# Optimization experiments

Hardware: AMD Instinct MI355X
Metric: run time of the kernel (lower is better)

The kernel has to match this reference:

```python
import jax, jax.numpy as jnp
import numpy as np

NUM_HEADS = 4
D_MODEL = 256
HEAD_DIM = D_MODEL // NUM_HEADS  # 64
B, N = 8, 2048


def _proj(x, W, b):
    # Conv1d with kernel_size=1 == pointwise linear over channel dim
    # x: [B, C_in, N], W: [C_out, C_in], b: [C_out]
    return jnp.einsum('oi,bin->bon', W, x) + b[None, :, None]


def setup_inputs() -> dict:
    key = jax.random.key(0)
    ks = jax.random.split(key, 11)
    s = 1.0 / np.sqrt(D_MODEL)
    return {
        'query': jax.random.normal(ks[0], (B, D_MODEL, N), jnp.float32),
        'key':   jax.random.normal(ks[1], (B, D_MODEL, N), jnp.float32),
        'value': jax.random.normal(ks[2], (B, D_MODEL, N), jnp.float32),
        'Wq': jax.random.normal(ks[3], (D_MODEL, D_MODEL), jnp.float32) * s,
        'bq': jax.random.normal(ks[4], (D_MODEL,), jnp.float32) * 0.01,
        'Wk': jax.random.normal(ks[5], (D_MODEL, D_MODEL), jnp.float32) * s,
        'bk': jax.random.normal(ks[6], (D_MODEL,), jnp.float32) * 0.01,
        'Wv': jax.random.normal(ks[7], (D_MODEL, D_MODEL), jnp.float32) * s,
        'bv': jax.random.normal(ks[8], (D_MODEL,), jnp.float32) * 0.01,
        'Wm': jax.random.normal(ks[9], (D_MODEL, D_MODEL), jnp.float32) * s,
        'bm': jax.random.normal(ks[10], (D_MODEL,), jnp.float32) * 0.01,
    }


def reference(query, key, value, Wq, bq, Wk, bk, Wv, bv, Wm, bm):
    b = query.shape[0]
    # project then split channels into (head_dim, num_heads): [B, d, h, N]
    q = _proj(query, Wq, bq).reshape(b, HEAD_DIM, NUM_HEADS, -1)
    k = _proj(key,   Wk, bk).reshape(b, HEAD_DIM, NUM_HEADS, -1)
    v = _proj(value, Wv, bv).reshape(b, HEAD_DIM, NUM_HEADS, -1)
    scale = 1.0 / jnp.sqrt(jnp.asarray(HEAD_DIM, q.dtype))
    scores = jnp.einsum('bdhn,bdhm->bhnm', q, k) * scale  # [B,H,N,N]
    prob = jax.nn.softmax(scores, axis=-1)
    x = jnp.einsum('bhnm,bdhm->bdhn', prob, v)  # [B,d,H,N]
    x = x.reshape(b, HEAD_DIM * NUM_HEADS, -1)  # [B, d_model, N]
    return _proj(x, Wm, bm)
```

## Files before the change

### kernel.cpp

```cpp
#include <hip/hip_runtime.h>
#include <math.h>


constexpr int BATCH  = 8;
constexpr int DMODEL = 256;
constexpr int SEQ    = 2048;
constexpr int HDIM   = 64;
constexpr int TN     = 128;
constexpr int TM     = 64;
constexpr int NJT    = SEQ / TM;

typedef _Float16 half4_t __attribute__((ext_vector_type(4)));
typedef _Float16 half8_t __attribute__((ext_vector_type(8)));
typedef float    float4_t __attribute__((ext_vector_type(4)));

static __device__ __forceinline__ void ld16_lds(const void* g, void* l) {
    __builtin_amdgcn_global_load_lds(
        (const __attribute__((address_space(1))) unsigned*)g,
        (__attribute__((address_space(3))) unsigned*)l, 16, 0, 0);
}

__global__ __launch_bounds__(256)
void prep_w(const float* __restrict__ Wq, const float* __restrict__ Wk,
            const float* __restrict__ Wv, const float* __restrict__ Wm,
            _Float16* __restrict__ wf)
{
    const int which = blockIdx.y;
    const float* src = which == 0 ? Wq : which == 1 ? Wk : which == 2 ? Wv : Wm;
    const int i = (blockIdx.x * 256 + threadIdx.x) * 4;
    const float4 v = *(const float4*)&src[i];
    half4_t o; o[0] = v.x; o[1] = v.y; o[2] = v.z; o[3] = v.w;
    *(half4_t*)&wf[(size_t)which * DMODEL * DMODEL + i] = o;
}

__global__ __launch_bounds__(256, 3)
void gemm_qkv(const _Float16* __restrict__ wf, const float* __restrict__ bq,
              const float* __restrict__ bk, const float* __restrict__ bv,
              const float* __restrict__ Xq, const float* __restrict__ Xk,
              const float* __restrict__ Xv, _Float16* __restrict__ qT,
              _Float16* __restrict__ kT, _Float16* __restrict__ vT)
{
    const int n0 = blockIdx.x * 64;
    const int proj = blockIdx.y >> 3, b = blockIdx.y & 7;
    const _Float16* W    = wf + (size_t)proj * DMODEL * DMODEL;
    const float*    bias = proj == 0 ? bq : proj == 1 ? bk : bv;
    const float*    X    = (proj == 0 ? Xq : proj == 1 ? Xk : Xv)
                           + (size_t)b * DMODEL * SEQ;
    const float qs = (proj == 0) ? 0.18033688011112042f : 1.0f;

    __shared__ __align__(16) char lds[50432];
    float*    T  = (float*)lds;
    _Float16* Xs = (_Float16*)(lds + 16640);
    _Float16* Tw = (_Float16*)lds;

    const int tid = threadIdx.x, tn = tid & 15, tc = tid >> 4;

    #pragma unroll
    for (int cc = 0; cc < 4; ++cc) {
        __syncthreads();
        #pragma unroll
        for (int i = 0; i < 4; ++i) {
            const int c = tc + 16 * i;
            const float4 v = *(const float4*)&X[(size_t)(cc * 64 + c) * SEQ + n0 + tn * 4];
            T[c * 65 + tn * 4 + 0] = v.x; T[c * 65 + tn * 4 + 1] = v.y;
            T[c * 65 + tn * 4 + 2] = v.z; T[c * 65 + tn * 4 + 3] = v.w;
        }
        __syncthreads();
        #pragma unroll
        for (int i = 0; i < 4; ++i) {
            const int n = tc + 16 * i;
            half4_t h4;
            #pragma unroll
            for (int j = 0; j < 4; ++j) h4[j] = (_Float16)T[(tn * 4 + j) * 65 + n];
            *(half4_t*)&Xs[n * 264 + cc * 64 + tn * 4] = h4;
        }
    }
    __syncthreads();

    const int w = tid >> 6, lane = tid & 63;
    const int lm = lane & 15, g = lane >> 4, g8 = g * 8;
    const int cw0 = w * 64;

    float4_t acc[4][4];
    #pragma unroll
    for (int mt = 0; mt < 4; ++mt)
        #pragma unroll
        for (int nt = 0; nt < 4; ++nt) acc[mt][nt] = (float4_t){0.f, 0.f, 0.f, 0.f};

    #pragma unroll
    for (int k0 = 0; k0 < DMODEL; k0 += 64) {
        half8_t a[4][2], bb[4][2];
        #pragma unroll
        for (int mt = 0; mt < 4; ++mt)
            #pragma unroll
            for (int kd = 0; kd < 2; ++kd)
                a[mt][kd] = *(const half8_t*)&W[(size_t)(cw0 + mt * 16 + lm) * DMODEL
                                                + k0 + kd * 32 + g8];
        #pragma unroll
        for (int nt = 0; nt < 4; ++nt)
            #pragma unroll
            for (int kd = 0; kd < 2; ++kd)
                bb[nt][kd] = *(const half8_t*)&Xs[(nt * 16 + lm) * 264
                                                  + k0 + kd * 32 + g8];
        #pragma unroll
        for (int kd = 0; kd < 2; ++kd)
            #pragma unroll
            for (int mt = 0; mt < 4; ++mt)
                #pragma unroll
                for (int nt = 0; nt < 4; ++nt)
                    acc[mt][nt] = __builtin_amdgcn_mfma_f32_16x16x32_f16(
                        a[mt][kd], bb[nt][kd], acc[mt][nt], 0, 0, 0);
    }
    __syncthreads();

    #pragma unroll
    for (int mt = 0; mt < 4; ++mt) {
        const float4 b4 = *(const float4*)&bias[cw0 + mt * 16 + g * 4];
        const float bb4[4] = {b4.x, b4.y, b4.z, b4.w};
        #pragma unroll
        for (int nt = 0; nt < 4; ++nt) {
            half4_t pk;
            #pragma unroll
            for (int r = 0; r < 4; ++r)
                pk[r] = (_Float16)((acc[mt][nt][r] + bb4[r]) * qs);
            *(half4_t*)&Tw[((w * 64 + nt * 16 + lm)) * 68 + mt * 16 + g * 4] = pk;
        }
    }

    if (proj < 2) {
        _Float16* dst = (proj == 0 ? qT : kT);
        const int h2 = lane >> 4, lml = lane & 15;
        #pragma unroll
        for (int it = 0; it < 4; ++it) {
            const int nl = it * 16 + lml;
            const int hs = (nl & 3) | (((nl >> 3) & 1) << 2);
            #pragma unroll
            for (int dc = 0; dc < 2; ++dc) {
                half8_t ch;
                #pragma unroll
                for (int e = 0; e < 8; ++e)
                    ch[e] = Tw[(w * 64 + nl) * 68 + 4 * (dc * 8 + e) + h2];
                const int chunk = (w * 2 + dc) ^ hs;
                *(half8_t*)&dst[((size_t)(b * 4 + h2) * SEQ + n0 + nl) * HDIM
                                + chunk * 8] = ch;
            }
        }
    } else {
        const int hh = lane & 3, dl = (lane >> 2) & 15;
        const int d = w * 16 + dl;
        const size_t rowbase =
            (((size_t)(b * 4 + hh) * NJT + (n0 >> 6)) * HDIM + d) * (size_t)TM;
        #pragma unroll
        for (int jc = 0; jc < 8; ++jc) {
            half8_t ch;
            #pragma unroll
            for (int e = 0; e < 8; ++e)
                ch[e] = Tw[(w * 64 + jc * 8 + e) * 68 + 4 * dl + hh];
            *(half8_t*)&vT[rowbase + ((jc ^ (dl & 7)) << 3)] = ch;
        }
    }
}

__global__ __launch_bounds__(256, 4)
void attn_f16(const _Float16* __restrict__ qT, const _Float16* __restrict__ kT,
              const _Float16* __restrict__ vT, _Float16* __restrict__ xa,
              _Float16* __restrict__ xb, float* __restrict__ rs)
{
    const int lid = blockIdx.x;
    const int work = (lid & 7) * 128 + (lid >> 3);
    const int bh = work >> 5, b = bh >> 2, h = bh & 3;
    const int jh = (work >> 4) & 1;
    const int ib = work & 15;
    const int tid = threadIdx.x, wid = tid >> 6, lane = tid & 63;
    const int lm = lane & 15, g = lane >> 4;
    const int i0 = ib * TN + wid * 32;

    __shared__ _Float16 Kb[2][TM * HDIM];
    __shared__ _Float16 Vb[2][TM * HDIM];

    const int hq = (lm & 3) | (((lm >> 3) & 1) << 2);
    const int hk = (lm & 3) | (((lm >> 2) & 1) << 2);
    const int rbase = 8 * (lm >> 2) + (lm & 3);

    half8_t bq[2][2];
    const _Float16* qbase = qT + (size_t)bh * SEQ * HDIM;
    #pragma unroll
    for (int rt = 0; rt < 2; ++rt)
        #pragma unroll
        for (int kd = 0; kd < 2; ++kd) {
            const int row = i0 + rt * 16 + lm;
            bq[rt][kd] = *(const half8_t*)(qbase + (size_t)row * HDIM
                                           + (((kd * 4 + g) ^ hq) << 3));
        }

    const char* kt = (const char*)(kT + ((size_t)bh * SEQ + jh * (SEQ / 2)) * HDIM);
    const char* vt = (const char*)(vT + ((size_t)bh * NJT + jh * 16) * TM * HDIM);

    float4_t o[2][4];
    float rsum[2][2] = {{0.f, 0.f}, {0.f, 0.f}};
    #pragma unroll
    for (int rt = 0; rt < 2; ++rt)
        #pragma unroll
        for (int dt = 0; dt < 4; ++dt) o[rt][dt] = (float4_t){0.f, 0.f, 0.f, 0.f};

    #define STAGE(jt, bu)                                                     \
        {                                                                     \
            const char* kg = kt + (size_t)(jt) * 8192;                        \
            const char* vg = vt + (size_t)(jt) * 8192;                        \
            _Pragma("unroll")                                                 \
            for (int p = 0; p < 2; ++p) {                                     \
                const int c = wid + p * 4;                                    \
                ld16_lds(kg + c * 1024 + lane * 16, (char*)&Kb[bu][0] + c * 1024); \
                ld16_lds(vg + c * 1024 + lane * 16, (char*)&Vb[bu][0] + c * 1024); \
            }                                                                 \
        }

    STAGE(0, 0);
    __syncthreads();

    for (int jt = 0; jt < 16; ++jt) {
        const int cur = jt & 1;
        if (jt + 1 < 16) STAGE(jt + 1, cur ^ 1);

        float4_t s[2][2][2];
        #pragma unroll
        for (int jb = 0; jb < 2; ++jb)
            #pragma unroll
            for (int u = 0; u < 2; ++u)
                #pragma unroll
                for (int rt = 0; rt < 2; ++rt)
                    s[jb][u][rt] = (float4_t){0.f, 0.f, 0.f, 0.f};
        #pragma unroll
        for (int kd = 0; kd < 2; ++kd)
            #pragma unroll
            for (int jb = 0; jb < 2; ++jb)
                #pragma unroll
                for (int u = 0; u < 2; ++u) {
                    const int jrow = jb * 32 + rbase + 4 * u;
                    const half8_t fk = *(const half8_t*)
                        &Kb[cur][jrow * HDIM + (((kd * 4 + g) ^ hk) << 3)];
                    #pragma unroll
                    for (int rt = 0; rt < 2; ++rt)
                        s[jb][u][rt] = __builtin_amdgcn_mfma_f32_16x16x32_f16(
                            fk, bq[rt][kd], s[jb][u][rt], 0, 0, 0);
                }

        half8_t ap[2][2];
        #pragma unroll
        for (int jb = 0; jb < 2; ++jb)
            #pragma unroll
            for (int rt = 0; rt < 2; ++rt) {
                half8_t p;
                #pragma unroll
                for (int r = 0; r < 4; ++r) {
                    const float e0 = __builtin_amdgcn_exp2f(s[jb][0][rt][r]);
                    const float e1 = __builtin_amdgcn_exp2f(s[jb][1][rt][r]);
                    rsum[jb][rt] += e0;
                    rsum[jb][rt] += e1;
                    p[r]     = (_Float16)e0;
                    p[r + 4] = (_Float16)e1;
                }
                ap[jb][rt] = p;
            }

        #pragma unroll
        for (int jb = 0; jb < 2; ++jb)
            #pragma unroll
            for (int dt = 0; dt < 4; ++dt) {
                const int d = dt * 16 + lm;
                const half8_t fv = *(const half8_t*)
                    &Vb[cur][d * TM + (((jb * 4 + g) ^ (lm & 7)) << 3)];
                #pragma unroll
                for (int rt = 0; rt < 2; ++rt)
                    o[rt][dt] = __builtin_amdgcn_mfma_f32_16x16x32_f16(
                        ap[jb][rt], fv, o[rt][dt], 0, 0, 0);
            }
        __syncthreads();
    }

    _Float16* xp = jh ? xb : xa;
    #pragma unroll
    for (int rt = 0; rt < 2; ++rt)
        #pragma unroll
        for (int dt = 0; dt < 4; ++dt) {
            const int c = 4 * (dt * 16 + lm) + h;
            #pragma unroll
            for (int r = 0; r < 4; ++r) {
                const int n = i0 + rt * 16 + 4 * g + r;
                xp[((size_t)b * SEQ + n) * DMODEL + c] = (_Float16)o[rt][dt][r];
            }
        }
    #pragma unroll
    for (int rt = 0; rt < 2; ++rt) {
        float v = rsum[0][rt] + rsum[1][rt];
        v += __shfl_xor(v, 16);
        v += __shfl_xor(v, 32);
        if (g == 0)
            rs[((size_t)jh * 32 + bh) * SEQ + i0 + rt * 16 + lm] = v;
    }
    #undef STAGE
}

__global__ __launch_bounds__(256)
void gemm_final(const _Float16* __restrict__ wm, const float* __restrict__ bias,
                const _Float16* __restrict__ xa, const _Float16* __restrict__ xb,
                const float* __restrict__ rs, float* __restrict__ out)
{
    const int n0 = blockIdx.x * 64, m0 = blockIdx.y * 128;
    const int b = blockIdx.z;
    const int tid = threadIdx.x, w = tid >> 6, lane = tid & 63;
    const int lm = lane & 15, g = lane >> 4, g8 = g * 8;
    const int cw0 = m0 + w * 32;

    const _Float16* Xa = xa + ((size_t)b * SEQ + n0) * DMODEL;
    const _Float16* Xb2 = xb + ((size_t)b * SEQ + n0) * DMODEL;

    half8_t pm[4];
    #pragma unroll
    for (int nt = 0; nt < 4; ++nt) {
        const int n = n0 + nt * 16 + lm;
        #pragma unroll
        for (int hh = 0; hh < 4; ++hh) {
            const float l = rs[(size_t)(b * 4 + hh) * SEQ + n]
                          + rs[(size_t)(32 + b * 4 + hh) * SEQ + n];
            const _Float16 iv = (_Float16)(1.0f / l);
            pm[nt][hh] = iv; pm[nt][hh + 4] = iv;
        }
    }

    float4_t acc[2][4];
    #pragma unroll
    for (int mt = 0; mt < 2; ++mt)
        #pragma unroll
        for (int nt = 0; nt < 4; ++nt) acc[mt][nt] = (float4_t){0.f, 0.f, 0.f, 0.f};

    #pragma unroll
    for (int k0 = 0; k0 < DMODEL; k0 += 64) {
        half8_t a[2][2], bb[4][2];
        #pragma unroll
        for (int mt = 0; mt < 2; ++mt)
            #pragma unroll
            for (int kd = 0; kd < 2; ++kd)
                a[mt][kd] = *(const half8_t*)&wm[(size_t)(cw0 + mt * 16 + lm) * DMODEL
                                                 + k0 + kd * 32 + g8];
        #pragma unroll
        for (int nt = 0; nt < 4; ++nt)
            #pragma unroll
            for (int kd = 0; kd < 2; ++kd) {
                const size_t off = (size_t)(nt * 16 + lm) * DMODEL + k0 + kd * 32 + g8;
                const half8_t va = *(const half8_t*)&Xa[off];
                const half8_t vb = *(const half8_t*)&Xb2[off];
                bb[nt][kd] = (va + vb) * pm[nt];
            }
        #pragma unroll
        for (int kd = 0; kd < 2; ++kd)
            #pragma unroll
            for (int mt = 0; mt < 2; ++mt)
                #pragma unroll
                for (int nt = 0; nt < 4; ++nt)
                    acc[mt][nt] = __builtin_amdgcn_mfma_f32_16x16x32_f16(
                        a[mt][kd], bb[nt][kd], acc[mt][nt], 0, 0, 0);
    }

    #pragma unroll
    for (int mt = 0; mt < 2; ++mt)
        #pragma unroll
        for (int r = 0; r < 4; ++r) {
            const int co = cw0 + mt * 16 + g * 4 + r;
            const float bv_ = bias[co];
            #pragma unroll
            for (int nt = 0; nt < 4; ++nt)
                out[((size_t)b * DMODEL + co) * SEQ + n0 + nt * 16 + lm] =
                    acc[mt][nt][r] + bv_;
        }
}

extern "C" void kernel_launch(void* const* d_in, const int* in_sizes, int n_in,
                              void* d_out, int out_size, void* d_ws, size_t ws_size,
                              hipStream_t stream) {
    const float* query = (const float*)d_in[0];
    const float* key_  = (const float*)d_in[1];
    const float* value = (const float*)d_in[2];
    const float* Wq = (const float*)d_in[3];  const float* bq = (const float*)d_in[4];
    const float* Wk = (const float*)d_in[5];  const float* bk = (const float*)d_in[6];
    const float* Wv = (const float*)d_in[7];  const float* bv = (const float*)d_in[8];
    const float* Wm = (const float*)d_in[9];  const float* bm = (const float*)d_in[10];
    float* out = (float*)d_out;

    const size_t bufElems = (size_t)BATCH * DMODEL * SEQ;
    _Float16* qT = (_Float16*)d_ws;
    _Float16* kT = qT + bufElems;
    _Float16* vT = kT + bufElems;
    _Float16* xa = vT + bufElems;
    _Float16* xb = xa + bufElems;
    _Float16* wf = xb + bufElems;
    float*    rsb = (float*)(wf + 4 * DMODEL * DMODEL);

    prep_w<<<dim3(DMODEL * DMODEL / 1024, 4), 256, 0, stream>>>(Wq, Wk, Wv, Wm, wf);
    gemm_qkv<<<dim3(SEQ / 64, 3 * BATCH), 256, 0, stream>>>(
        wf, bq, bk, bv, query, key_, value, qT, kT, vT);
    attn_f16<<<dim3(1024), 256, 0, stream>>>(qT, kT, vT, xa, xb, rsb);
    gemm_final<<<dim3(SEQ / 64, 2, BATCH), 256, 0, stream>>>(
        wf + (size_t)3 * DMODEL * DMODEL, bm, xa, xb, rsb, out);
}
```

Baseline: 188.1 us.

## Triple-buffer K/V tiles with single barrier, setprio around MFMA, fdot2 row sums

Moves the attention loop from double to triple buffering of the K/V LDS tiles, so one explicit vmcnt wait plus a single s_barrier per iteration replaces the two __syncthreads, and loads can run further ahead. The loop is fully unrolled. MFMA sections are wrapped in s_setprio to favour matrix issue. Row sums are now accumulated with fdot2 over the fp16-rounded probabilities instead of separate fp32 adds. LDS use grows by half, so the occupancy hint drops from 4 to 3 blocks per CU, and the row sum now comes from rounded values.

```diff
diff --git a/kernel.cpp b/kernel.cpp
--- a/kernel.cpp
+++ b/kernel.cpp
@@ -10,6 +10,7 @@
 constexpr int TM     = 64;
 constexpr int NJT    = SEQ / TM;
 
+typedef _Float16 half2_t __attribute__((ext_vector_type(2)));
 typedef _Float16 half4_t __attribute__((ext_vector_type(4)));
 typedef _Float16 half8_t __attribute__((ext_vector_type(8)));
 typedef float    float4_t __attribute__((ext_vector_type(4)));
@@ -161,7 +162,7 @@
     }
 }
 
-__global__ __launch_bounds__(256, 4)
+__global__ __launch_bounds__(256, 3)
 void attn_f16(const _Float16* __restrict__ qT, const _Float16* __restrict__ kT,
               const _Float16* __restrict__ vT, _Float16* __restrict__ xa,
               _Float16* __restrict__ xb, float* __restrict__ rs)
@@ -175,8 +176,8 @@
     const int lm = lane & 15, g = lane >> 4;
     const int i0 = ib * TN + wid * 32;
 
-    __shared__ _Float16 Kb[2][TM * HDIM];
-    __shared__ _Float16 Vb[2][TM * HDIM];
+    __shared__ _Float16 Kb[3][TM * HDIM];
+    __shared__ _Float16 Vb[3][TM * HDIM];
 
     const int hq = (lm & 3) | (((lm >> 3) & 1) << 2);
     const int hk = (lm & 3) | (((lm >> 2) & 1) << 2);
@@ -202,6 +203,8 @@
     for (int rt = 0; rt < 2; ++rt)
         #pragma unroll
         for (int dt = 0; dt < 4; ++dt) o[rt][dt] = (float4_t){0.f, 0.f, 0.f, 0.f};
+
+    const half2_t one2 = {(_Float16)1.f, (_Float16)1.f};
 
     #define STAGE(jt, bu)                                                     \
         {                                                                     \
@@ -216,11 +219,19 @@
         }
 
     STAGE(0, 0);
-    __syncthreads();
-
+
+    int cur = 0;
+    #pragma unroll
     for (int jt = 0; jt < 16; ++jt) {
-        const int cur = jt & 1;
-        if (jt + 1 < 16) STAGE(jt + 1, cur ^ 1);
+        const int nxt = (cur == 2) ? 0 : cur + 1;
+        if (jt + 1 < 16) {
+            STAGE(jt + 1, nxt);
+            asm volatile("s_waitcnt vmcnt(4)" ::: "memory");
+        } else {
+            asm volatile("s_waitcnt vmcnt(0)" ::: "memory");
+        }
+        __builtin_amdgcn_s_barrier();
+        asm volatile("" ::: "memory");
 
         float4_t s[2][2][2];
         #pragma unroll
@@ -230,6 +241,7 @@
                 #pragma unroll
                 for (int rt = 0; rt < 2; ++rt)
                     s[jb][u][rt] = (float4_t){0.f, 0.f, 0.f, 0.f};
+        __builtin_amdgcn_s_setprio(1);
         #pragma unroll
         for (int kd = 0; kd < 2; ++kd)
             #pragma unroll
@@ -244,6 +256,7 @@
                         s[jb][u][rt] = __builtin_amdgcn_mfma_f32_16x16x32_f16(
                             fk, bq[rt][kd], s[jb][u][rt], 0, 0, 0);
                 }
+        __builtin_amdgcn_s_setprio(0);
 
         half8_t ap[2][2];
         #pragma unroll
@@ -253,16 +266,19 @@
                 half8_t p;
                 #pragma unroll
                 for (int r = 0; r < 4; ++r) {
-                    const float e0 = __builtin_amdgcn_exp2f(s[jb][0][rt][r]);
-                    const float e1 = __builtin_amdgcn_exp2f(s[jb][1][rt][r]);
-                    rsum[jb][rt] += e0;
-                    rsum[jb][rt] += e1;
-                    p[r]     = (_Float16)e0;
-                    p[r + 4] = (_Float16)e1;
+                    p[r]     = (_Float16)__builtin_amdgcn_exp2f(s[jb][0][rt][r]);
+                    p[r + 4] = (_Float16)__builtin_amdgcn_exp2f(s[jb][1][rt][r]);
                 }
                 ap[jb][rt] = p;
+                #pragma unroll
+                for (int q = 0; q < 4; ++q) {
+                    half2_t h2; h2[0] = p[2 * q]; h2[1] = p[2 * q + 1];
+                    rsum[jb][rt] = __builtin_amdgcn_fdot2(h2, one2,
+                                                          rsum[jb][rt], false);
+                }
             }
 
+        __builtin_amdgcn_s_setprio(1);
         #pragma unroll
         for (int jb = 0; jb < 2; ++jb)
             #pragma unroll
@@ -275,7 +291,8 @@
                     o[rt][dt] = __builtin_amdgcn_mfma_f32_16x16x32_f16(
                         ap[jb][rt], fv, o[rt][dt], 0, 0, 0);
             }
-        __syncthreads();
+        __builtin_amdgcn_s_setprio(0);
+        cur = nxt;
     }
 
     _Float16* xp = jh ? xb : xa;
```

After: 210.0 us. +11.6%, slower.
